# Kernel optimization log

Hardware: AMD Instinct MI355X
Metric: run time of the kernel (lower is better)

## Reference

```python
import jax, jax.numpy as jnp
import numpy as np

H = 16        # query heads
KV = 4        # key/value heads
HD = 64       # head dim
BASE = 10000.0
SCALE = HD ** (-0.5) * 0.8


def setup_inputs() -> dict:
    key = jax.random.key(0)
    ks = jax.random.split(key, 5)
    B, S, D = 2, 4096, 1024
    return {
        "hidden_states": jax.random.normal(ks[0], (B, S, D), dtype=jnp.float32),
        "wq": jax.random.normal(ks[1], (D, H * HD), dtype=jnp.float32) * (D ** -0.5),
        "wk": jax.random.normal(ks[2], (D, KV * HD), dtype=jnp.float32) * (D ** -0.5),
        "wv": jax.random.normal(ks[3], (D, KV * HD), dtype=jnp.float32) * (D ** -0.5),
        "wo": jax.random.normal(ks[4], (H * HD, D), dtype=jnp.float32) * ((H * HD) ** -0.5),
    }


def _rope_tables(seq_len, dtype):
    inv_freq = 1.0 / (BASE ** (jnp.arange(0, HD, 2, dtype=jnp.float32) / HD))
    t = jnp.arange(seq_len, dtype=jnp.float32)
    freqs = t[:, None] * inv_freq[None, :]            # [S, HD/2]
    emb = jnp.concatenate([freqs, freqs], axis=-1)    # [S, HD]
    return jnp.cos(emb).astype(dtype), jnp.sin(emb).astype(dtype)


def _rotate_half(x):
    x1, x2 = x[..., : HD // 2], x[..., HD // 2 :]
    return jnp.concatenate([-x2, x1], axis=-1)


def reference(hidden_states, wq, wk, wv, wo):
    B, S, D = hidden_states.shape
    G = H // KV
    q = (hidden_states @ wq).reshape(B, S, H, HD).transpose(0, 2, 1, 3)   # [B,H,S,HD]
    k = (hidden_states @ wk).reshape(B, S, KV, HD).transpose(0, 2, 1, 3)  # [B,KV,S,HD]
    v = (hidden_states @ wv).reshape(B, S, KV, HD).transpose(0, 2, 1, 3)
    cos, sin = _rope_tables(S, q.dtype)               # [S,HD] each
    cos = cos[None, None]                             # [1,1,S,HD]
    sin = sin[None, None]
    q = q * cos + _rotate_half(q) * sin
    k = k * cos + _rotate_half(k) * sin
    k = jnp.repeat(k, G, axis=1)                      # [B,H,S,HD]
    v = jnp.repeat(v, G, axis=1)
    scores = jnp.einsum("bhqd,bhkd->bhqk", q, k) * SCALE
    probs = jax.nn.softmax(scores.astype(jnp.float32), axis=-1).astype(q.dtype)
    out = jnp.einsum("bhqk,bhkd->bhqd", probs, v)     # [B,H,S,HD]
    out = out.transpose(0, 2, 1, 3).reshape(B, S, H * HD)
    return out @ wo
```

## Files before the change

### kernel.cpp

```cpp
#include <hip/hip_runtime.h>
#include <hip/hip_fp16.h>
#include <math.h>

typedef _Float16 f16;
typedef _Float16 half8 __attribute__((ext_vector_type(8)));
typedef _Float16 half4v __attribute__((ext_vector_type(4)));
typedef _Float16 half2v __attribute__((ext_vector_type(2)));
typedef float f32x4 __attribute__((ext_vector_type(4)));
typedef float f32x16 __attribute__((ext_vector_type(16)));
typedef unsigned uint2v __attribute__((ext_vector_type(2)));

#define NB 2
#define NS 4096
#define ND 1024
#define NH 16
#define NKV 4
#define NHD 64
#define ATT_SCALE2 0.14426950408889634f

__global__ __launch_bounds__(256) void wprep_k(
    const float* __restrict__ wq, const float* __restrict__ wk,
    const float* __restrict__ wv, const float* __restrict__ wo,
    f16* __restrict__ Bt, f16* __restrict__ Wot)
{
  __shared__ f16 tile[64][72];
  int bx = blockIdx.x, by = blockIdx.y;
  const float* src; int ldn, colbase, nbase; f16* dst;
  if (bx < 24) {
    int n0 = bx * 64;
    if (n0 < 1024)      { src = wq; ldn = 1024; colbase = n0; }
    else if (n0 < 1280) { src = wk; ldn = 256;  colbase = n0 - 1024; }
    else                { src = wv; ldn = 256;  colbase = n0 - 1280; }
    dst = Bt; nbase = n0;
  } else {
    src = wo; ldn = 1024; colbase = (bx - 24) * 64; dst = Wot; nbase = (bx - 24) * 64;
  }
  int tid = threadIdx.x;
  int kr = tid >> 4;
  int nc = (tid & 15) * 4;
  #pragma unroll
  for (int i = 0; i < 4; ++i) {
    int k = by * 64 + kr + i * 16;
    float4 v = *reinterpret_cast<const float4*>(src + (size_t)k * ldn + colbase + nc);
    tile[nc + 0][kr + i * 16] = (f16)v.x;
    tile[nc + 1][kr + i * 16] = (f16)v.y;
    tile[nc + 2][kr + i * 16] = (f16)v.z;
    tile[nc + 3][kr + i * 16] = (f16)v.w;
  }
  __syncthreads();
  int nl = tid >> 2;
  int kb = (tid & 3) * 16;
  half8 a = *reinterpret_cast<const half8*>(&tile[nl][kb]);
  half8 b = *reinterpret_cast<const half8*>(&tile[nl][kb + 8]);
  f16* o = dst + (size_t)(nbase + nl) * 1024 + by * 64 + kb;
  *reinterpret_cast<half8*>(o) = a;
  *reinterpret_cast<half8*>(o + 8) = b;
}

template<int MODE>
__global__ __launch_bounds__(256) void gemm_k(
    const float* __restrict__ Af32, const f16* __restrict__ Af16,
    const f16* __restrict__ Bt,
    f16* __restrict__ q_h, f16* __restrict__ k_h, f16* __restrict__ vT_h,
    float* __restrict__ outp)
{
  __shared__ f16 As[128 * 32];
  __shared__ f16 Bs[128 * 32];
  int tid = threadIdx.x;
  int lane = tid & 63, w = tid >> 6;
  int wr = w >> 1, wc = w & 1;
  int g = lane >> 4, lr = lane & 15;
  int m0 = blockIdx.y * 128, n0 = blockIdx.x * 128;

  f32x4 acc[4][4] = {};

  int ar = tid >> 1;
  int ac = (tid & 1) * 16;

  for (int k0 = 0; k0 < ND; k0 += 32) {
    if (MODE == 0) {
      const float* Ap = Af32 + (size_t)(m0 + ar) * ND + k0 + ac;
      #pragma unroll
      for (int i = 0; i < 4; ++i) {
        float4 v = *reinterpret_cast<const float4*>(Ap + i * 4);
        int col = ac + i * 4;
        int slot = (col >> 3) ^ (ar & 3);
        half4v hv = { (f16)v.x, (f16)v.y, (f16)v.z, (f16)v.w };
        *reinterpret_cast<half4v*>(&As[ar * 32 + slot * 8 + (col & 7)]) = hv;
      }
    } else {
      const f16* Ap = Af16 + (size_t)(m0 + ar) * ND + k0 + ac;
      half8 v0 = *reinterpret_cast<const half8*>(Ap);
      half8 v1 = *reinterpret_cast<const half8*>(Ap + 8);
      int s0 = (ac >> 3) ^ (ar & 3);
      int s1 = ((ac >> 3) + 1) ^ (ar & 3);
      *reinterpret_cast<half8*>(&As[ar * 32 + s0 * 8]) = v0;
      *reinterpret_cast<half8*>(&As[ar * 32 + s1 * 8]) = v1;
    }
    {
      const f16* Bp = Bt + (size_t)(n0 + ar) * ND + k0 + ac;
      half8 v0 = *reinterpret_cast<const half8*>(Bp);
      half8 v1 = *reinterpret_cast<const half8*>(Bp + 8);
      int s0 = (ac >> 3) ^ (ar & 3);
      int s1 = ((ac >> 3) + 1) ^ (ar & 3);
      *reinterpret_cast<half8*>(&Bs[ar * 32 + s0 * 8]) = v0;
      *reinterpret_cast<half8*>(&Bs[ar * 32 + s1 * 8]) = v1;
    }
    __syncthreads();
    half8 af[4], bf[4];
    #pragma unroll
    for (int mt = 0; mt < 4; ++mt) {
      int row = wr * 64 + mt * 16 + lr;
      af[mt] = *reinterpret_cast<const half8*>(&As[row * 32 + (g ^ (row & 3)) * 8]);
    }
    #pragma unroll
    for (int nt = 0; nt < 4; ++nt) {
      int row = wc * 64 + nt * 16 + lr;
      bf[nt] = *reinterpret_cast<const half8*>(&Bs[row * 32 + (g ^ (row & 3)) * 8]);
    }
    #pragma unroll
    for (int mt = 0; mt < 4; ++mt)
      #pragma unroll
      for (int nt = 0; nt < 4; ++nt)
        acc[mt][nt] = __builtin_amdgcn_mfma_f32_16x16x32_f16(af[mt], bf[nt], acc[mt][nt], 0, 0, 0);
    __syncthreads();
  }

  #pragma unroll
  for (int mt = 0; mt < 4; ++mt)
    #pragma unroll
    for (int nt = 0; nt < 4; ++nt)
      #pragma unroll
      for (int r = 0; r < 4; ++r) {
        int m = m0 + wr * 64 + mt * 16 + g * 4 + r;
        int n = n0 + wc * 64 + nt * 16 + lr;
        float val = acc[mt][nt][r];
        if (MODE == 0) {
          int b = m >> 12, s = m & (NS - 1);
          f16 hv = (f16)val;
          if (n < 1024)      q_h[(((size_t)b * NH + (n >> 6)) * NS + s) * NHD + (n & 63)] = hv;
          else if (n < 1280) { int nn = n - 1024; k_h[(((size_t)b * NKV + (nn >> 6)) * NS + s) * NHD + (nn & 63)] = hv; }
          else               { int nn = n - 1280; vT_h[(((size_t)b * NKV + (nn >> 6)) * NHD + (nn & 63)) * NS + s] = hv; }
        } else {
          outp[(size_t)m * ND + n] = val;
        }
      }
}

__global__ __launch_bounds__(256) void rope_k(f16* __restrict__ q_h, f16* __restrict__ k_h)
{
  __shared__ float cs[16][33], sn[16][33];
  int b = blockIdx.y;
  int s0 = blockIdx.x * 16;
  int tid = threadIdx.x;
  for (int idx = tid; idx < 512; idx += 256) {
    int sl = idx >> 5, d = idx & 31;
    double inv = exp((double)d * -0.28782313662425575);
    double ang = (double)(s0 + sl) * inv;
    cs[sl][d] = (float)cos(ang);
    sn[sl][d] = (float)sin(ang);
  }
  __syncthreads();
  for (int p = tid; p < 512 * 20; p += 256) {
    int u = p >> 9; int rem = p & 511; int sl = rem >> 5; int d = rem & 31;
    f16* ptr;
    if (u < NH) ptr = q_h + (((size_t)b * NH + u) * NS + s0 + sl) * NHD;
    else        ptr = k_h + (((size_t)b * NKV + (u - NH)) * NS + s0 + sl) * NHD;
    float x1 = (float)ptr[d], x2 = (float)ptr[d + 32];
    float c = cs[sl][d], si = sn[sl][d];
    ptr[d]      = (f16)(x1 * c - x2 * si);
    ptr[d + 32] = (f16)(x2 * c + x1 * si);
  }
}

__global__ __launch_bounds__(512) void attn_k(
    const f16* __restrict__ q_h, const f16* __restrict__ k_h,
    const f16* __restrict__ vT_h, f16* __restrict__ attn_h)
{
  __shared__ f16 Ks[2][64 * 64];
  __shared__ f16 Vs[2][64 * 64];
  int tid = threadIdx.x;
  int lane = tid & 63, w = tid >> 6;
  int hi = lane >> 5, qr = lane & 31;
  int bh = blockIdx.x; int b = bh >> 4, h = bh & 15, kvh = h >> 2;
  int q0 = blockIdx.y * 256 + w * 32;

  const f16* qptr = q_h + (((size_t)b * NH + h) * NS + q0 + qr) * NHD + hi * 8;
  half8 qf[4];
  #pragma unroll
  for (int ks = 0; ks < 4; ++ks)
    qf[ks] = *reinterpret_cast<const half8*>(qptr + 16 * ks);

  const f16* kbase = k_h + ((size_t)b * NKV + kvh) * NS * NHD;
  const f16* vbase = vT_h + ((size_t)b * NKV + kvh) * NHD * NS;

  f32x16 accO[2] = {};
  float m_run = 0.0f;
  float l_lane = 0.f;

  int srow = tid >> 3;
  int scol = (tid & 7) * 8;
  int sslot = ((scol >> 3) ^ (srow & 7)) * 8;
  int qs = qr & 7;

  {
    half8 kv0 = *reinterpret_cast<const half8*>(kbase + (size_t)srow * NHD + scol);
    half8 vv0 = *reinterpret_cast<const half8*>(vbase + (size_t)srow * NS + scol);
    *reinterpret_cast<half8*>(&Ks[0][srow * 64 + sslot]) = kv0;
    *reinterpret_cast<half8*>(&Vs[0][srow * 64 + sslot]) = vv0;
  }

  const half2v ones2 = { (f16)1.0f, (f16)1.0f };

  int cur = 0;
  for (int t = 0; t < 64; ++t) {
    __syncthreads();
    int tn = (t < 63) ? t + 1 : t;
    int kt2 = tn * 64;
    half8 kreg = *reinterpret_cast<const half8*>(kbase + (size_t)(kt2 + srow) * NHD + scol);
    half8 vreg = *reinterpret_cast<const half8*>(vbase + (size_t)srow * NS + kt2 + scol);

    const f16* Kc = &Ks[cur][0];
    const f16* Vc = &Vs[cur][0];

    f32x16 sc0 = {}, sc1 = {};
    #pragma unroll
    for (int ks = 0; ks < 4; ++ks) {
      int cs = 2 * ks + hi;
      half8 kf0 = *reinterpret_cast<const half8*>(&Kc[qr * 64 + ((cs ^ qs) << 3)]);
      half8 kf1 = *reinterpret_cast<const half8*>(&Kc[(32 + qr) * 64 + ((cs ^ qs) << 3)]);
      __builtin_amdgcn_s_setprio(1);
      sc0 = __builtin_amdgcn_mfma_f32_32x32x16_f16(kf0, qf[ks], sc0, 0, 0, 0);
      sc1 = __builtin_amdgcn_mfma_f32_32x32x16_f16(kf1, qf[ks], sc1, 0, 0, 0);
      __builtin_amdgcn_s_setprio(0);
    }

    unsigned wrd[2][4][2];
    float l0 = 0.f, l1 = 0.f;
    #pragma unroll
    for (int e = 0; e < 4; ++e)
      #pragma unroll
      for (int p = 0; p < 2; ++p) {
        float a0 = exp2f(fmaf(sc0[e * 4 + p * 2], ATT_SCALE2, -m_run));
        float a1 = exp2f(fmaf(sc0[e * 4 + p * 2 + 1], ATT_SCALE2, -m_run));
        unsigned u0 = __builtin_bit_cast(unsigned, __builtin_amdgcn_cvt_pkrtz(a0, a1));
        wrd[0][e][p] = u0;
        l0 = __builtin_amdgcn_fdot2(__builtin_bit_cast(half2v, u0), ones2, l0, false);
        float b0 = exp2f(fmaf(sc1[e * 4 + p * 2], ATT_SCALE2, -m_run));
        float b1 = exp2f(fmaf(sc1[e * 4 + p * 2 + 1], ATT_SCALE2, -m_run));
        unsigned u1 = __builtin_bit_cast(unsigned, __builtin_amdgcn_cvt_pkrtz(b0, b1));
        wrd[1][e][p] = u1;
        l1 = __builtin_amdgcn_fdot2(__builtin_bit_cast(half2v, u1), ones2, l1, false);
      }
    float ltile = l0 + l1;
    l_lane += ltile;

    #pragma unroll
    for (int ks = 0; ks < 4; ++ks) {
      int kb = ks >> 1, e0 = 2 * (ks & 1);
      uint2v s0 = __builtin_amdgcn_permlane32_swap(wrd[kb][e0][0], wrd[kb][e0 + 1][0], false, false);
      uint2v s1 = __builtin_amdgcn_permlane32_swap(wrd[kb][e0][1], wrd[kb][e0 + 1][1], false, false);
      union { unsigned u[4]; half8 h; } pfu;
      pfu.u[0] = s0[0]; pfu.u[1] = s1[0]; pfu.u[2] = s0[1]; pfu.u[3] = s1[1];
      int cs = 2 * ks + hi;
      half8 vf0 = *reinterpret_cast<const half8*>(&Vc[qr * 64 + ((cs ^ qs) << 3)]);
      half8 vf1 = *reinterpret_cast<const half8*>(&Vc[(32 + qr) * 64 + ((cs ^ qs) << 3)]);
      __builtin_amdgcn_s_setprio(1);
      accO[0] = __builtin_amdgcn_mfma_f32_32x32x16_f16(vf0, pfu.h, accO[0], 0, 0, 0);
      accO[1] = __builtin_amdgcn_mfma_f32_32x32x16_f16(vf1, pfu.h, accO[1], 0, 0, 0);
      __builtin_amdgcn_s_setprio(0);
    }

    if (__any(ltile > 16384.0f)) {
      const float alpha = 0x1p-16f;
      #pragma unroll
      for (int db = 0; db < 2; ++db)
        #pragma unroll
        for (int i = 0; i < 16; ++i) accO[db][i] *= alpha;
      l_lane *= alpha;
      m_run += 16.0f;
    }

    *reinterpret_cast<half8*>(&Ks[cur ^ 1][srow * 64 + sslot]) = kreg;
    *reinterpret_cast<half8*>(&Vs[cur ^ 1][srow * 64 + sslot]) = vreg;
    cur ^= 1;
  }

  float l_tot = l_lane + __shfl_xor(l_lane, 32);
  float inv_l = 1.0f / l_tot;
  f16* obase = attn_h + ((size_t)b * NS + q0 + qr) * ND + h * NHD;
  #pragma unroll
  for (int db = 0; db < 2; ++db)
    #pragma unroll
    for (int e = 0; e < 4; ++e) {
      half4v ov = { (f16)(accO[db][e * 4 + 0] * inv_l), (f16)(accO[db][e * 4 + 1] * inv_l),
                    (f16)(accO[db][e * 4 + 2] * inv_l), (f16)(accO[db][e * 4 + 3] * inv_l) };
      *reinterpret_cast<half4v*>(obase + db * 32 + e * 8 + hi * 4) = ov;
    }
}

extern "C" void kernel_launch(void* const* d_in, const int* in_sizes, int n_in,
                              void* d_out, int out_size, void* d_ws, size_t ws_size,
                              hipStream_t stream)
{
  (void)in_sizes; (void)n_in; (void)out_size; (void)ws_size;
  const float* hs = (const float*)d_in[0];
  const float* wq = (const float*)d_in[1];
  const float* wk = (const float*)d_in[2];
  const float* wv = (const float*)d_in[3];
  const float* wo = (const float*)d_in[4];
  float* outp = (float*)d_out;

  f16* q_h    = (f16*)d_ws;
  f16* k_h    = q_h    + (size_t)NB * NH * NS * NHD;
  f16* vT_h   = k_h    + (size_t)NB * NKV * NS * NHD;
  f16* attn_h = vT_h   + (size_t)NB * NKV * NS * NHD;
  f16* Bt     = attn_h + (size_t)NB * NS * ND;
  f16* Wot    = Bt     + (size_t)1536 * 1024;

  wprep_k<<<dim3(40, 16), 256, 0, stream>>>(wq, wk, wv, wo, Bt, Wot);
  gemm_k<0><<<dim3(12, 64), 256, 0, stream>>>(hs, nullptr, Bt, q_h, k_h, vT_h, nullptr);
  rope_k<<<dim3(256, 2), 256, 0, stream>>>(q_h, k_h);
  attn_k<<<dim3(32, 16), 512, 0, stream>>>(q_h, k_h, vT_h, attn_h);
  gemm_k<1><<<dim3(8, 64), 256, 0, stream>>>(nullptr, attn_h, Wot, nullptr, nullptr, nullptr, outp);
}
```

Baseline: 328.1 us.

## Use direct global-to-LDS loads and interleave softmax with PV MFMAs in attention

The K/V tile prefetch now uses global_load_lds, which writes straight into shared memory with a pre-swizzled source address, instead of staging through registers and storing to LDS at the end of each iteration. Softmax exponentiation is split into chunks interleaved with the PV MFMA steps, so VALU exp work can overlap matrix-core work. Launch bounds now ask for higher occupancy. The risks are register pressure from the occupancy hint, and an LDS-ready hazard: the final iteration reloads into the buffer currently being read, and correctness depends on vmcnt waits before the barrier.

```diff
diff --git a/kernel.cpp b/kernel.cpp
--- a/kernel.cpp
+++ b/kernel.cpp
@@ -17,6 +17,10 @@
 #define NKV 4
 #define NHD 64
 #define ATT_SCALE2 0.14426950408889634f
+
+#define GL16(gp, lp) __builtin_amdgcn_global_load_lds( \
+    (const __attribute__((address_space(1))) unsigned int*)(const void*)(gp), \
+    (__attribute__((address_space(3))) unsigned int*)(void*)(lp), 16, 0, 0)
 
 __global__ __launch_bounds__(256) void wprep_k(
     const float* __restrict__ wq, const float* __restrict__ wk,
@@ -173,7 +177,7 @@
   }
 }
 
-__global__ __launch_bounds__(512) void attn_k(
+__global__ __launch_bounds__(512, 6) void attn_k(
     const f16* __restrict__ q_h, const f16* __restrict__ k_h,
     const f16* __restrict__ vT_h, f16* __restrict__ attn_h)
 {
@@ -199,26 +203,55 @@
   float l_lane = 0.f;
 
   int srow = tid >> 3;
-  int scol = (tid & 7) * 8;
-  int sslot = ((scol >> 3) ^ (srow & 7)) * 8;
+  int gswz = (((tid & 7) ^ ((tid >> 3) & 7)) << 3);
   int qs = qr & 7;
 
   {
-    half8 kv0 = *reinterpret_cast<const half8*>(kbase + (size_t)srow * NHD + scol);
-    half8 vv0 = *reinterpret_cast<const half8*>(vbase + (size_t)srow * NS + scol);
-    *reinterpret_cast<half8*>(&Ks[0][srow * 64 + sslot]) = kv0;
-    *reinterpret_cast<half8*>(&Vs[0][srow * 64 + sslot]) = vv0;
+    GL16(kbase + (size_t)srow * NHD + gswz, &Ks[0][w * 512]);
+    GL16(vbase + (size_t)srow * NS + gswz, &Vs[0][w * 512]);
   }
 
   const half2v ones2 = { (f16)1.0f, (f16)1.0f };
+
+  unsigned wrd[2][4][2];
+
+#define SMCHUNK(KB, SC, E, LACC) do { \
+    float a0_ = exp2f(fmaf((SC)[(E) * 4 + 0], ATT_SCALE2, -m_run)); \
+    float a1_ = exp2f(fmaf((SC)[(E) * 4 + 1], ATT_SCALE2, -m_run)); \
+    unsigned u0_ = __builtin_bit_cast(unsigned, __builtin_amdgcn_cvt_pkrtz(a0_, a1_)); \
+    wrd[KB][E][0] = u0_; \
+    LACC = __builtin_amdgcn_fdot2(__builtin_bit_cast(half2v, u0_), ones2, LACC, false); \
+    float a2_ = exp2f(fmaf((SC)[(E) * 4 + 2], ATT_SCALE2, -m_run)); \
+    float a3_ = exp2f(fmaf((SC)[(E) * 4 + 3], ATT_SCALE2, -m_run)); \
+    unsigned u1_ = __builtin_bit_cast(unsigned, __builtin_amdgcn_cvt_pkrtz(a2_, a3_)); \
+    wrd[KB][E][1] = u1_; \
+    LACC = __builtin_amdgcn_fdot2(__builtin_bit_cast(half2v, u1_), ones2, LACC, false); \
+  } while (0)
+
+#define PVSTEP(KS) do { \
+    int kb_ = (KS) >> 1, e0_ = 2 * ((KS) & 1); \
+    uint2v s0_ = __builtin_amdgcn_permlane32_swap(wrd[kb_][e0_][0], wrd[kb_][e0_ + 1][0], false, false); \
+    uint2v s1_ = __builtin_amdgcn_permlane32_swap(wrd[kb_][e0_][1], wrd[kb_][e0_ + 1][1], false, false); \
+    union { unsigned u[4]; half8 h; } pfu_; \
+    pfu_.u[0] = s0_[0]; pfu_.u[1] = s1_[0]; pfu_.u[2] = s0_[1]; pfu_.u[3] = s1_[1]; \
+    int cs_ = 2 * (KS) + hi; \
+    half8 vf0_ = *reinterpret_cast<const half8*>(&Vc[qr * 64 + ((cs_ ^ qs) << 3)]); \
+    half8 vf1_ = *reinterpret_cast<const half8*>(&Vc[(32 + qr) * 64 + ((cs_ ^ qs) << 3)]); \
+    __builtin_amdgcn_s_setprio(1); \
+    accO[0] = __builtin_amdgcn_mfma_f32_32x32x16_f16(vf0_, pfu_.h, accO[0], 0, 0, 0); \
+    accO[1] = __builtin_amdgcn_mfma_f32_32x32x16_f16(vf1_, pfu_.h, accO[1], 0, 0, 0); \
+    __builtin_amdgcn_s_setprio(0); \
+  } while (0)
 
   int cur = 0;
   for (int t = 0; t < 64; ++t) {
     __syncthreads();
-    int tn = (t < 63) ? t + 1 : t;
-    int kt2 = tn * 64;
-    half8 kreg = *reinterpret_cast<const half8*>(kbase + (size_t)(kt2 + srow) * NHD + scol);
-    half8 vreg = *reinterpret_cast<const half8*>(vbase + (size_t)srow * NS + kt2 + scol);
+    {
+      int tn = (t < 63) ? t + 1 : t;
+      int kt2 = tn * 64;
+      GL16(kbase + (size_t)(kt2 + srow) * NHD + gswz, &Ks[cur ^ 1][w * 512]);
+      GL16(vbase + (size_t)srow * NS + kt2 + gswz, &Vs[cur ^ 1][w * 512]);
+    }
 
     const f16* Kc = &Ks[cur][0];
     const f16* Vc = &Vs[cur][0];
@@ -235,41 +268,22 @@
       __builtin_amdgcn_s_setprio(0);
     }
 
-    unsigned wrd[2][4][2];
     float l0 = 0.f, l1 = 0.f;
-    #pragma unroll
-    for (int e = 0; e < 4; ++e)
-      #pragma unroll
-      for (int p = 0; p < 2; ++p) {
-        float a0 = exp2f(fmaf(sc0[e * 4 + p * 2], ATT_SCALE2, -m_run));
-        float a1 = exp2f(fmaf(sc0[e * 4 + p * 2 + 1], ATT_SCALE2, -m_run));
-        unsigned u0 = __builtin_bit_cast(unsigned, __builtin_amdgcn_cvt_pkrtz(a0, a1));
-        wrd[0][e][p] = u0;
-        l0 = __builtin_amdgcn_fdot2(__builtin_bit_cast(half2v, u0), ones2, l0, false);
-        float b0 = exp2f(fmaf(sc1[e * 4 + p * 2], ATT_SCALE2, -m_run));
-        float b1 = exp2f(fmaf(sc1[e * 4 + p * 2 + 1], ATT_SCALE2, -m_run));
-        unsigned u1 = __builtin_bit_cast(unsigned, __builtin_amdgcn_cvt_pkrtz(b0, b1));
-        wrd[1][e][p] = u1;
-        l1 = __builtin_amdgcn_fdot2(__builtin_bit_cast(half2v, u1), ones2, l1, false);
-      }
+    SMCHUNK(0, sc0, 0, l0);
+    SMCHUNK(0, sc0, 1, l0);
+    PVSTEP(0);
+    SMCHUNK(0, sc0, 2, l0);
+    SMCHUNK(0, sc0, 3, l0);
+    PVSTEP(1);
+    SMCHUNK(1, sc1, 0, l1);
+    SMCHUNK(1, sc1, 1, l1);
+    PVSTEP(2);
+    SMCHUNK(1, sc1, 2, l1);
+    SMCHUNK(1, sc1, 3, l1);
+    PVSTEP(3);
+
     float ltile = l0 + l1;
     l_lane += ltile;
-
-    #pragma unroll
-    for (int ks = 0; ks < 4; ++ks) {
-      int kb = ks >> 1, e0 = 2 * (ks & 1);
-      uint2v s0 = __builtin_amdgcn_permlane32_swap(wrd[kb][e0][0], wrd[kb][e0 + 1][0], false, false);
-      uint2v s1 = __builtin_amdgcn_permlane32_swap(wrd[kb][e0][1], wrd[kb][e0 + 1][1], false, false);
-      union { unsigned u[4]; half8 h; } pfu;
-      pfu.u[0] = s0[0]; pfu.u[1] = s1[0]; pfu.u[2] = s0[1]; pfu.u[3] = s1[1];
-      int cs = 2 * ks + hi;
-      half8 vf0 = *reinterpret_cast<const half8*>(&Vc[qr * 64 + ((cs ^ qs) << 3)]);
-      half8 vf1 = *reinterpret_cast<const half8*>(&Vc[(32 + qr) * 64 + ((cs ^ qs) << 3)]);
-      __builtin_amdgcn_s_setprio(1);
-      accO[0] = __builtin_amdgcn_mfma_f32_32x32x16_f16(vf0, pfu.h, accO[0], 0, 0, 0);
-      accO[1] = __builtin_amdgcn_mfma_f32_32x32x16_f16(vf1, pfu.h, accO[1], 0, 0, 0);
-      __builtin_amdgcn_s_setprio(0);
-    }
 
     if (__any(ltile > 16384.0f)) {
       const float alpha = 0x1p-16f;
@@ -281,8 +295,6 @@
       m_run += 16.0f;
     }
 
-    *reinterpret_cast<half8*>(&Ks[cur ^ 1][srow * 64 + sslot]) = kreg;
-    *reinterpret_cast<half8*>(&Vs[cur ^ 1][srow * 64 + sslot]) = vreg;
     cur ^= 1;
   }
 
@@ -297,6 +309,8 @@
                     (f16)(accO[db][e * 4 + 2] * inv_l), (f16)(accO[db][e * 4 + 3] * inv_l) };
       *reinterpret_cast<half4v*>(obase + db * 32 + e * 8 + hi * 4) = ov;
     }
+#undef SMCHUNK
+#undef PVSTEP
 }
 
 extern "C" void kernel_launch(void* const* d_in, const int* in_sizes, int n_in,
```

Result: slower. 741.7 us (+126.1%).

## Split attention KV sequence across wave pairs with in-block softmax merge

Applied to the files above, without the earlier changes.

Each block now covers 128 queries instead of 256, and pairs of waves split the key/value sequence in half. Each wave processes 32-key tiles, and the two partial outputs are merged at the end through shared memory using a running-max rescale. The grid doubles to raise parallelism and occupancy, and the launch bound asks for higher occupancy. In exchange there is an extra merge step, a padded V layout in shared memory, and more K/V global traffic per query.

```diff
diff --git a/kernel.cpp b/kernel.cpp
--- a/kernel.cpp
+++ b/kernel.cpp
@@ -173,17 +173,21 @@
   }
 }
 
-__global__ __launch_bounds__(512) void attn_k(
+__global__ __launch_bounds__(512, 8) void attn_k(
     const f16* __restrict__ q_h, const f16* __restrict__ k_h,
     const f16* __restrict__ vT_h, f16* __restrict__ attn_h)
 {
-  __shared__ f16 Ks[2][64 * 64];
-  __shared__ f16 Vs[2][64 * 64];
+  __shared__ __align__(16) char smem_raw[36864];
+  f16* Kst = (f16*)smem_raw;
+  f16* Vst = (f16*)(smem_raw + 16384);
+
   int tid = threadIdx.x;
   int lane = tid & 63, w = tid >> 6;
   int hi = lane >> 5, qr = lane & 31;
+  int g = w >> 1, s = w & 1;
   int bh = blockIdx.x; int b = bh >> 4, h = bh & 15, kvh = h >> 2;
-  int q0 = blockIdx.y * 256 + w * 32;
+  int q0 = blockIdx.y * 128 + g * 32;
+  int soff = s * 2048;
 
   const f16* qptr = q_h + (((size_t)b * NH + h) * NS + q0 + qr) * NHD + hi * 8;
   half8 qf[4];
@@ -198,16 +202,18 @@
   float m_run = 0.0f;
   float l_lane = 0.f;
 
-  int srow = tid >> 3;
-  int scol = (tid & 7) * 8;
-  int sslot = ((scol >> 3) ^ (srow & 7)) * 8;
-  int qs = qr & 7;
+  int ts = ((w >> 1) << 6) | lane;
+  int ksr = ts >> 3, ksc = ts & 7;
+  int kslot = ((ksc ^ (ksr & 7)) << 3);
+  int vsr = ts >> 2, vsc = ts & 3;
+  int vslot = ((vsc ^ (vsr & 3)) << 3);
+  int qs7 = qr & 7, qs3 = qr & 3;
 
   {
-    half8 kv0 = *reinterpret_cast<const half8*>(kbase + (size_t)srow * NHD + scol);
-    half8 vv0 = *reinterpret_cast<const half8*>(vbase + (size_t)srow * NS + scol);
-    *reinterpret_cast<half8*>(&Ks[0][srow * 64 + sslot]) = kv0;
-    *reinterpret_cast<half8*>(&Vs[0][srow * 64 + sslot]) = vv0;
+    half8 k0 = *reinterpret_cast<const half8*>(kbase + (size_t)(soff + ksr) * NHD + ksc * 8);
+    half8 v0 = *reinterpret_cast<const half8*>(vbase + (size_t)vsr * NS + soff + vsc * 8);
+    *reinterpret_cast<half8*>(&Kst[s * 2048 + ksr * 64 + kslot]) = k0;
+    *reinterpret_cast<half8*>(&Vst[s * 2560 + vsr * 40 + vslot]) = v0;
   }
 
   const half2v ones2 = { (f16)1.0f, (f16)1.0f };
@@ -216,62 +222,54 @@
   for (int t = 0; t < 64; ++t) {
     __syncthreads();
     int tn = (t < 63) ? t + 1 : t;
-    int kt2 = tn * 64;
-    half8 kreg = *reinterpret_cast<const half8*>(kbase + (size_t)(kt2 + srow) * NHD + scol);
-    half8 vreg = *reinterpret_cast<const half8*>(vbase + (size_t)srow * NS + kt2 + scol);
-
-    const f16* Kc = &Ks[cur][0];
-    const f16* Vc = &Vs[cur][0];
-
-    f32x16 sc0 = {}, sc1 = {};
+    int r0 = soff + tn * 32;
+    half8 kreg = *reinterpret_cast<const half8*>(kbase + (size_t)(r0 + ksr) * NHD + ksc * 8);
+    half8 vreg = *reinterpret_cast<const half8*>(vbase + (size_t)vsr * NS + r0 + vsc * 8);
+
+    const f16* Kc = &Kst[(cur * 2 + s) * 2048];
+    const f16* Vc = &Vst[(cur * 2 + s) * 2560];
+
+    f32x16 sc = {};
     #pragma unroll
     for (int ks = 0; ks < 4; ++ks) {
       int cs = 2 * ks + hi;
-      half8 kf0 = *reinterpret_cast<const half8*>(&Kc[qr * 64 + ((cs ^ qs) << 3)]);
-      half8 kf1 = *reinterpret_cast<const half8*>(&Kc[(32 + qr) * 64 + ((cs ^ qs) << 3)]);
+      half8 kf = *reinterpret_cast<const half8*>(&Kc[qr * 64 + ((cs ^ qs7) << 3)]);
       __builtin_amdgcn_s_setprio(1);
-      sc0 = __builtin_amdgcn_mfma_f32_32x32x16_f16(kf0, qf[ks], sc0, 0, 0, 0);
-      sc1 = __builtin_amdgcn_mfma_f32_32x32x16_f16(kf1, qf[ks], sc1, 0, 0, 0);
+      sc = __builtin_amdgcn_mfma_f32_32x32x16_f16(kf, qf[ks], sc, 0, 0, 0);
       __builtin_amdgcn_s_setprio(0);
     }
 
-    unsigned wrd[2][4][2];
-    float l0 = 0.f, l1 = 0.f;
+    unsigned wrd[4][2];
+    float l0 = 0.f;
     #pragma unroll
     for (int e = 0; e < 4; ++e)
       #pragma unroll
       for (int p = 0; p < 2; ++p) {
-        float a0 = exp2f(fmaf(sc0[e * 4 + p * 2], ATT_SCALE2, -m_run));
-        float a1 = exp2f(fmaf(sc0[e * 4 + p * 2 + 1], ATT_SCALE2, -m_run));
+        float a0 = exp2f(fmaf(sc[e * 4 + p * 2], ATT_SCALE2, -m_run));
+        float a1 = exp2f(fmaf(sc[e * 4 + p * 2 + 1], ATT_SCALE2, -m_run));
         unsigned u0 = __builtin_bit_cast(unsigned, __builtin_amdgcn_cvt_pkrtz(a0, a1));
-        wrd[0][e][p] = u0;
+        wrd[e][p] = u0;
         l0 = __builtin_amdgcn_fdot2(__builtin_bit_cast(half2v, u0), ones2, l0, false);
-        float b0 = exp2f(fmaf(sc1[e * 4 + p * 2], ATT_SCALE2, -m_run));
-        float b1 = exp2f(fmaf(sc1[e * 4 + p * 2 + 1], ATT_SCALE2, -m_run));
-        unsigned u1 = __builtin_bit_cast(unsigned, __builtin_amdgcn_cvt_pkrtz(b0, b1));
-        wrd[1][e][p] = u1;
-        l1 = __builtin_amdgcn_fdot2(__builtin_bit_cast(half2v, u1), ones2, l1, false);
       }
-    float ltile = l0 + l1;
-    l_lane += ltile;
-
-    #pragma unroll
-    for (int ks = 0; ks < 4; ++ks) {
-      int kb = ks >> 1, e0 = 2 * (ks & 1);
-      uint2v s0 = __builtin_amdgcn_permlane32_swap(wrd[kb][e0][0], wrd[kb][e0 + 1][0], false, false);
-      uint2v s1 = __builtin_amdgcn_permlane32_swap(wrd[kb][e0][1], wrd[kb][e0 + 1][1], false, false);
+    l_lane += l0;
+
+    #pragma unroll
+    for (int ks = 0; ks < 2; ++ks) {
+      int e0 = 2 * ks;
+      uint2v s0 = __builtin_amdgcn_permlane32_swap(wrd[e0][0], wrd[e0 + 1][0], false, false);
+      uint2v s1 = __builtin_amdgcn_permlane32_swap(wrd[e0][1], wrd[e0 + 1][1], false, false);
       union { unsigned u[4]; half8 h; } pfu;
       pfu.u[0] = s0[0]; pfu.u[1] = s1[0]; pfu.u[2] = s0[1]; pfu.u[3] = s1[1];
-      int cs = 2 * ks + hi;
-      half8 vf0 = *reinterpret_cast<const half8*>(&Vc[qr * 64 + ((cs ^ qs) << 3)]);
-      half8 vf1 = *reinterpret_cast<const half8*>(&Vc[(32 + qr) * 64 + ((cs ^ qs) << 3)]);
+      int sl = 2 * ks + hi;
+      half8 vf0 = *reinterpret_cast<const half8*>(&Vc[qr * 40 + ((sl ^ qs3) << 3)]);
+      half8 vf1 = *reinterpret_cast<const half8*>(&Vc[(32 + qr) * 40 + ((sl ^ qs3) << 3)]);
       __builtin_amdgcn_s_setprio(1);
       accO[0] = __builtin_amdgcn_mfma_f32_32x32x16_f16(vf0, pfu.h, accO[0], 0, 0, 0);
       accO[1] = __builtin_amdgcn_mfma_f32_32x32x16_f16(vf1, pfu.h, accO[1], 0, 0, 0);
       __builtin_amdgcn_s_setprio(0);
     }
 
-    if (__any(ltile > 16384.0f)) {
+    if (__any(l0 > 16384.0f)) {
       const float alpha = 0x1p-16f;
       #pragma unroll
       for (int db = 0; db < 2; ++db)
@@ -281,22 +279,45 @@
       m_run += 16.0f;
     }
 
-    *reinterpret_cast<half8*>(&Ks[cur ^ 1][srow * 64 + sslot]) = kreg;
-    *reinterpret_cast<half8*>(&Vs[cur ^ 1][srow * 64 + sslot]) = vreg;
+    *reinterpret_cast<half8*>(&Kst[((cur ^ 1) * 2 + s) * 2048 + ksr * 64 + kslot]) = kreg;
+    *reinterpret_cast<half8*>(&Vst[((cur ^ 1) * 2 + s) * 2560 + vsr * 40 + vslot]) = vreg;
     cur ^= 1;
   }
 
-  float l_tot = l_lane + __shfl_xor(l_lane, 32);
-  float inv_l = 1.0f / l_tot;
-  f16* obase = attn_h + ((size_t)b * NS + q0 + qr) * ND + h * NHD;
-  #pragma unroll
-  for (int db = 0; db < 2; ++db)
-    #pragma unroll
-    for (int e = 0; e < 4; ++e) {
-      half4v ov = { (f16)(accO[db][e * 4 + 0] * inv_l), (f16)(accO[db][e * 4 + 1] * inv_l),
-                    (f16)(accO[db][e * 4 + 2] * inv_l), (f16)(accO[db][e * 4 + 3] * inv_l) };
-      *reinterpret_cast<half4v*>(obase + db * 32 + e * 8 + hi * 4) = ov;
-    }
+  __syncthreads();
+  float* xO = (float*)smem_raw;
+  float* lm = (float*)(smem_raw + 32768);
+  if (s == 1) {
+    #pragma unroll
+    for (int i = 0; i < 32; ++i)
+      xO[(g * 32 + i) * 64 + lane] = accO[i >> 4][i & 15];
+    lm[(g * 2 + 0) * 64 + lane] = l_lane;
+    lm[(g * 2 + 1) * 64 + lane] = m_run;
+  }
+  __syncthreads();
+  if (s == 0) {
+    float l_b = lm[(g * 2 + 0) * 64 + lane];
+    float m_b = lm[(g * 2 + 1) * 64 + lane];
+    float mmax = fmaxf(m_run, m_b);
+    float a0 = exp2f(m_run - mmax), a1 = exp2f(m_b - mmax);
+    #pragma unroll
+    for (int db = 0; db < 2; ++db)
+      #pragma unroll
+      for (int i = 0; i < 16; ++i)
+        accO[db][i] = a0 * accO[db][i] + a1 * xO[(g * 32 + db * 16 + i) * 64 + lane];
+    float l_c = a0 * l_lane + a1 * l_b;
+    float l_tot = l_c + __shfl_xor(l_c, 32);
+    float inv_l = 1.0f / l_tot;
+    f16* obase = attn_h + ((size_t)b * NS + q0 + qr) * ND + h * NHD;
+    #pragma unroll
+    for (int db = 0; db < 2; ++db)
+      #pragma unroll
+      for (int e = 0; e < 4; ++e) {
+        half4v ov = { (f16)(accO[db][e * 4 + 0] * inv_l), (f16)(accO[db][e * 4 + 1] * inv_l),
+                      (f16)(accO[db][e * 4 + 2] * inv_l), (f16)(accO[db][e * 4 + 3] * inv_l) };
+        *reinterpret_cast<half4v*>(obase + db * 32 + e * 8 + hi * 4) = ov;
+      }
+  }
 }
 
 extern "C" void kernel_launch(void* const* d_in, const int* in_sizes, int n_in,
@@ -321,6 +342,6 @@
   wprep_k<<<dim3(40, 16), 256, 0, stream>>>(wq, wk, wv, wo, Bt, Wot);
   gemm_k<0><<<dim3(12, 64), 256, 0, stream>>>(hs, nullptr, Bt, q_h, k_h, vT_h, nullptr);
   rope_k<<<dim3(256, 2), 256, 0, stream>>>(q_h, k_h);
-  attn_k<<<dim3(32, 16), 512, 0, stream>>>(q_h, k_h, vT_h, attn_h);
+  attn_k<<<dim3(32, 32), 512, 0, stream>>>(q_h, k_h, vT_h, attn_h);
   gemm_k<1><<<dim3(8, 64), 256, 0, stream>>>(nullptr, attn_h, Wot, nullptr, nullptr, nullptr, outp);
 }
```

New measurement: 996.6 us. 3.04x slower.
